# Kernel optimization log

Measured on AMD Instinct MI355X. Metric: run time of the kernel, lower is better.

## Reference

```python
import jax, jax.numpy as jnp
import numpy as np

H = 64
N_NODES = 12000
N_EDGES = 50000


def setup_inputs() -> dict:
    key = jax.random.key(0)
    ks = jax.random.split(key, 16)
    s = 1.0 / np.sqrt(H)
    inp = {
        "node": jax.random.normal(ks[0], (N_NODES, H), jnp.float32),
        "edge": jax.random.normal(ks[1], (N_EDGES, H), jnp.float32),
        "hidden_feats": jax.random.normal(ks[2], (N_NODES, H), jnp.float32),
        "src": jax.random.randint(ks[3], (N_EDGES,), 0, N_NODES, jnp.int32),
        "dst": jax.random.randint(ks[4], (N_EDGES,), 0, N_NODES, jnp.int32),
        # edge_network: Linear(H, 2H) -> ReLU -> Linear(2H, H*H)
        "W1": jax.random.uniform(ks[5], (2 * H, H), jnp.float32, -s, s),
        "b1": jax.random.uniform(ks[6], (2 * H,), jnp.float32, -s, s),
        "W2": jax.random.uniform(ks[7], (H * H, 2 * H), jnp.float32, -1 / np.sqrt(2 * H), 1 / np.sqrt(2 * H)),
        "b2": jax.random.uniform(ks[8], (H * H,), jnp.float32, -1 / np.sqrt(2 * H), 1 / np.sqrt(2 * H)),
        # GRUCell params (torch layout: [3H, H], gate order r,z,n)
        "W_ih": jax.random.uniform(ks[9], (3 * H, H), jnp.float32, -s, s),
        "W_hh": jax.random.uniform(ks[10], (3 * H, H), jnp.float32, -s, s),
        "b_ih": jax.random.uniform(ks[11], (3 * H,), jnp.float32, -s, s),
        "b_hh": jax.random.uniform(ks[12], (3 * H,), jnp.float32, -s, s),
        # LayerNorm params
        "gamma": jnp.ones((H,), jnp.float32),
        "beta": jnp.zeros((H,), jnp.float32),
    }
    return inp


def _gru_cell(x, h, W_ih, W_hh, b_ih, b_hh):
    gi = x @ W_ih.T + b_ih  # [N, 3H]
    gh = h @ W_hh.T + b_hh  # [N, 3H]
    r = jax.nn.sigmoid(gi[:, :H] + gh[:, :H])
    z = jax.nn.sigmoid(gi[:, H:2 * H] + gh[:, H:2 * H])
    n = jnp.tanh(gi[:, 2 * H:] + r * gh[:, 2 * H:])
    return (1.0 - z) * n + z * h


def reference(node, edge, hidden_feats, src, dst, W1, b1, W2, b2,
              W_ih, W_hh, b_ih, b_hh, gamma, beta):
    n_nodes = node.shape[0]
    # edge network -> per-edge [H,H] weight matrices
    eh = jax.nn.relu(edge @ W1.T + b1)                      # [E, 2H]
    Wedge = (eh @ W2.T + b2).reshape(-1, H, H)              # [E, H, H]
    # gather src feats, per-edge matmul (row-vector @ matrix), scatter-sum to dst
    msg = jnp.einsum('eh,ehk->ek', node[src], Wedge)        # [E, H]
    agg = jax.ops.segment_sum(msg, dst, num_segments=n_nodes)  # [N, H]
    new_node_feats = jax.nn.relu(agg)
    out = _gru_cell(new_node_feats, hidden_feats, W_ih, W_hh, b_ih, b_hh)
    # LayerNorm (eps=1e-5)
    mu = jnp.mean(out, axis=-1, keepdims=True)
    var = jnp.var(out, axis=-1, keepdims=True)
    out = (out - mu) * jax.lax.rsqrt(var + 1e-5) * gamma + beta
    return out
```

## Files before the change

kernel.cpp:

```cpp
#include <hip/hip_runtime.h>

#define H 64
#define NEDGE 50000
#define NNODE 12000
#define EPAD 50176

typedef _Float16 f16;
typedef _Float16 h8 __attribute__((ext_vector_type(8)));
typedef float f4 __attribute__((ext_vector_type(4)));

#define O_EDGEH 0ull
#define O_W2G   6422528ull
#define O_W1G   7471104ull
#define O_WG    7487488ull
#define O_NB    7553024ull
#define O_AGG   10625024ull

__device__ __forceinline__ void async16(const void* g, void* l) {
  __builtin_amdgcn_global_load_lds((const __attribute__((address_space(1))) void*)g,
                                   (__attribute__((address_space(3))) void*)l, 16, 0, 0);
}

__global__ __launch_bounds__(256) void k_prep(const float* __restrict__ edge, const float* __restrict__ W1,
                                              const float* __restrict__ W2, const float* __restrict__ b2,
                                              const float* __restrict__ node,
                                              const float* __restrict__ Wih, const float* __restrict__ Whh,
                                              f16* __restrict__ edgeh, f16* __restrict__ w1g, f16* __restrict__ w2g,
                                              f16* __restrict__ wg, float* __restrict__ nb) {
  int bid = blockIdx.x;
  int t = threadIdx.x;
  if (bid < 1568) {
    long id8 = (long)bid * 256 + t;
    long e = id8 >> 3;
    int c = (int)(id8 & 7) * 8;
    h8 o = {};
    if (e < NEDGE) {
      const float* p = edge + e * 64 + c;
      f4 v0 = *(const f4*)p, v1 = *(const f4*)(p + 4);
#pragma unroll
      for (int j = 0; j < 4; ++j) { o[j] = (f16)v0[j]; o[4 + j] = (f16)v1[j]; }
    }
    *(h8*)(edgeh + e * 64 + c) = o;
    return;
  }
  if (bid < 3616) {
    int id = (bid - 1568) * 256 + t;
    int ii = id & 7, l = (id >> 3) & 63, t4 = (id >> 9) & 3, s = (id >> 11) & 3, h = id >> 13;
    int n = t4 * 16 + (l & 15), j = s * 32 + ((l >> 4) << 3) + ii;
    w2g[id] = (f16)W2[(h * 64 + n) * 128 + j];
    return;
  }
  if (bid < 3648) {
    int id = (bid - 3616) * 256 + t;
    int ii = id & 7, l = (id >> 3) & 63, tt = (id >> 9) & 7, s = id >> 12;
    int n = tt * 16 + (l & 15), k = s * 32 + ((l >> 4) << 3) + ii;
    w1g[id] = (f16)W1[n * 64 + k];
    return;
  }
  if (bid < 3776) {
    int id = (bid - 3648) * 256 + t;
    int ii = id & 7, l = (id >> 3) & 63, tt = (id >> 9) & 15, s = id >> 13;
    int k = s * 32 + ((l >> 4) << 3) + ii, n = tt * 16 + (l & 15);
    float v;
    if (n < 128) v = (k < 64) ? Wih[n * 64 + k] : Whh[n * 64 + (k - 64)];
    else if (n < 192) v = (k < 64) ? Wih[n * 64 + k] : 0.f;
    else v = (k < 64) ? 0.f : Whh[(n - 64) * 64 + (k - 64)];
    wg[id] = (f16)v;
    return;
  }
  __shared__ float bs[64][65];
  __shared__ float xs[64][65];
  int n0 = (bid - 3776) * 64;
#pragma unroll
  for (int it = 0; it < 16; ++it) {
    int idx = t + it * 256;
    int rr = idx >> 6, cc = idx & 63;
    bs[rr][cc] = b2[idx];
    int nn = n0 + rr;
    xs[rr][cc] = (nn < NNODE) ? node[(long)nn * 64 + cc] : 0.f;
  }
  __syncthreads();
  int f0 = (t & 15) * 4, e0 = (t >> 4) * 4;
  float acc[4][4] = {};
#pragma unroll 4
  for (int k = 0; k < 64; ++k) {
    f4 w = *(const f4*)&bs[k][f0];
#pragma unroll
    for (int i = 0; i < 4; ++i) {
      float x = xs[e0 + i][k];
      acc[i][0] = fmaf(x, w[0], acc[i][0]); acc[i][1] = fmaf(x, w[1], acc[i][1]);
      acc[i][2] = fmaf(x, w[2], acc[i][2]); acc[i][3] = fmaf(x, w[3], acc[i][3]);
    }
  }
#pragma unroll
  for (int i = 0; i < 4; ++i) {
    int nn = n0 + e0 + i;
    if (nn < NNODE)
#pragma unroll
      for (int j = 0; j < 4; ++j) nb[(long)nn * 64 + f0 + j] = acc[i][j];
  }
}

__global__ __launch_bounds__(256, 3) void k_msg(const float* __restrict__ node,
                                                const int* __restrict__ src, const int* __restrict__ dst,
                                                const f16* __restrict__ edgeh, const f16* __restrict__ w1g,
                                                const f16* __restrict__ w2g, const float* __restrict__ b1,
                                                const float* __restrict__ nbt, float* __restrict__ agg) {
  __shared__ __align__(16) f16 est[64 * 8 * 8];
  __shared__ __align__(16) f16 eh_s[64 * 16 * 8];
  __shared__ __align__(16) f16 vT2[64 * 8 * 8];
  __shared__ int ssrc[64];
  __shared__ int sdst[64];
  __shared__ float b1s[128];

  int t = threadIdx.x;
  int e_base = blockIdx.x * 64;

  if (t < 64) {
    int eg = e_base + t;
    bool valid = eg < NEDGE;
    ssrc[t] = valid ? src[eg] : 0;
    sdst[t] = valid ? dst[eg] : 0;
  }
  if (t >= 128) b1s[t - 128] = b1[t - 128];
  {
    const char* ehb = (const char*)edgeh;
#pragma unroll
    for (int r = 0; r < 2; ++r) {
      int idx = r * 256 + t;
      int e = idx >> 3, c1 = idx & 7;
      int c = c1 ^ (e & 7);
      async16(ehb + ((long)(e_base + e) * 8 + c) * 16, (char*)est + idx * 16);
    }
  }
  {
    int e = t >> 2, q = t & 3;
    int eg = e_base + e;
    int si = (eg < NEDGE) ? src[eg] : 0;
    const f4* nr = (const f4*)(node + (long)si * 64 + q * 16);
    f4 a0 = nr[0], a1 = nr[1], a2 = nr[2], a3 = nr[3];
    h8 p0, p1;
#pragma unroll
    for (int m = 0; m < 4; ++m) {
      p0[m] = (f16)a0[m]; p0[4 + m] = (f16)a1[m];
      p1[m] = (f16)a2[m]; p1[4 + m] = (f16)a3[m];
    }
    int g0 = (q * 2) ^ (e & 7), g1 = (q * 2 + 1) ^ (e & 7);
    *(h8*)(vT2 + (e * 8 + g0) * 8) = p0;
    *(h8*)(vT2 + (e * 8 + g1) * 8) = p1;
  }
  __syncthreads();

  int wave = t >> 6, lane = t & 63;
  int l15 = lane & 15, lq = lane >> 4;

  {
    h8 afr[4][2];
#pragma unroll
    for (int g = 0; g < 4; ++g) {
      int e = g * 16 + l15;
#pragma unroll
      for (int s = 0; s < 2; ++s) {
        int c = (s * 4 + lq) ^ (e & 7);
        afr[g][s] = *(const h8*)(est + (e * 8 + c) * 8);
      }
    }
    h8 bfr[2][2];
#pragma unroll
    for (int s = 0; s < 2; ++s)
#pragma unroll
      for (int j = 0; j < 2; ++j)
        bfr[s][j] = *(const h8*)(w1g + ((s * 8 + wave * 2 + j) * 64 + lane) * 8);
    f4 acc_eh[4][2];
#pragma unroll
    for (int g = 0; g < 4; ++g) { acc_eh[g][0] = (f4){0,0,0,0}; acc_eh[g][1] = (f4){0,0,0,0}; }
#pragma unroll
    for (int s = 0; s < 2; ++s)
#pragma unroll
      for (int g = 0; g < 4; ++g)
#pragma unroll
        for (int j = 0; j < 2; ++j)
          acc_eh[g][j] = __builtin_amdgcn_mfma_f32_16x16x32_f16(afr[g][s], bfr[s][j], acc_eh[g][j], 0, 0, 0);
#pragma unroll
    for (int g = 0; g < 4; ++g)
#pragma unroll
      for (int j = 0; j < 2; ++j) {
        int n = wave * 32 + j * 16 + l15;
        int jg = n >> 3;
#pragma unroll
        for (int r = 0; r < 4; ++r) {
          int e = g * 16 + lq * 4 + r;
          float val = fmaxf(acc_eh[g][j][r] + b1s[n], 0.f);
          eh_s[(e * 16 + (jg ^ (e & 15))) * 8 + (n & 7)] = (f16)val;
        }
      }
  }
  __syncthreads();

  h8 ehreg[4][4];
#pragma unroll
  for (int g = 0; g < 4; ++g) {
    int e = g * 16 + l15;
#pragma unroll
    for (int s = 0; s < 4; ++s) {
      int jg = (s * 4 + lq) ^ (e & 15);
      ehreg[g][s] = *(const h8*)(eh_s + (e * 16 + jg) * 8);
    }
  }

  f4 acc[4];
#pragma unroll
  for (int g = 0; g < 4; ++g) acc[g] = (f4){0.f, 0.f, 0.f, 0.f};

  const char* w2b = (const char*)w2g + wave * 1024 + lane * 16;
  h8 cur0 = *(const h8*)(w2b);
  h8 cur1 = *(const h8*)(w2b + 4096);
  h8 cur2 = *(const h8*)(w2b + 8192);
  h8 cur3 = *(const h8*)(w2b + 12288);

#pragma unroll 1
  for (int hb = 0; hb < 8; ++hb) {
    h8 vh8[4];
#pragma unroll
    for (int g = 0; g < 4; ++g) {
      int e = g * 16 + l15;
      vh8[g] = *(const h8*)(vT2 + (e * 8 + (hb ^ (e & 7))) * 8);
    }
#pragma unroll
    for (int hh = 0; hh < 8; ++hh) {
      int h = hb * 8 + hh;
      const char* gp = w2b + (long)(h + 1) * 16384;
      h8 pf0 = *(const h8*)(gp);
      h8 pf1 = *(const h8*)(gp + 4096);
      h8 pf2 = *(const h8*)(gp + 8192);
      h8 pf3 = *(const h8*)(gp + 12288);
      f16 vs;
#pragma unroll
      for (int g = 0; g < 4; ++g) {
        vs = vh8[g][hh];
        h8 a = ehreg[g][0] * vs;
        acc[g] = __builtin_amdgcn_mfma_f32_16x16x32_f16(a, cur0, acc[g], 0, 0, 0);
        a = ehreg[g][1] * vs;
        acc[g] = __builtin_amdgcn_mfma_f32_16x16x32_f16(a, cur1, acc[g], 0, 0, 0);
        a = ehreg[g][2] * vs;
        acc[g] = __builtin_amdgcn_mfma_f32_16x16x32_f16(a, cur2, acc[g], 0, 0, 0);
        a = ehreg[g][3] * vs;
        acc[g] = __builtin_amdgcn_mfma_f32_16x16x32_f16(a, cur3, acc[g], 0, 0, 0);
      }
      cur0 = pf0; cur1 = pf1; cur2 = pf2; cur3 = pf3;
    }
  }

  int n = wave * 16 + l15;
#pragma unroll
  for (int g = 0; g < 4; ++g)
#pragma unroll
    for (int r = 0; r < 4; ++r) {
      int el = g * 16 + lq * 4 + r;
      if (e_base + el < NEDGE) {
        float v = acc[g][r] + nbt[(long)ssrc[el] * 64 + n];
        atomicAdd(&agg[(long)sdst[el] * 64 + n], v);
      }
    }
}

__global__ __launch_bounds__(256) void k_node(const float* __restrict__ agg, const float* __restrict__ hid,
                                              const f16* __restrict__ wg,
                                              const float* __restrict__ bih, const float* __restrict__ bhh,
                                              const float* __restrict__ gamma, const float* __restrict__ beta,
                                              float* __restrict__ out) {
  __shared__ __align__(16) f16 xh_s[128 * 136];
  __shared__ float bsum[128], bin_s[64], bhn_s[64], gam_s[64], bet_s[64];
  int t = threadIdx.x;
  int n0 = blockIdx.x * 128;

  if (t < 128) bsum[t] = bih[t] + bhh[t];
  else if (t < 192) bin_s[t - 128] = bih[t];
  else bhn_s[t - 192] = bhh[t - 64];
  if (t < 64) gam_s[t] = gamma[t];
  else if (t < 128) bet_s[t - 64] = beta[t - 64];

  {
    int m = t >> 1, half = t & 1;
    int mg = n0 + m;
    bool vld = mg < NNODE;
    const float* sp = half ? (hid + (long)mg * 64) : (agg + (long)mg * 64);
#pragma unroll
    for (int jj = 0; jj < 8; ++jj) {
      f4 v0 = {0,0,0,0}, v1 = {0,0,0,0};
      if (vld) { v0 = *(const f4*)(sp + jj * 8); v1 = *(const f4*)(sp + jj * 8 + 4); }
      h8 pk;
#pragma unroll
      for (int m2 = 0; m2 < 4; ++m2) {
        pk[m2] = (f16)(half ? v0[m2] : fmaxf(v0[m2], 0.f));
        pk[4 + m2] = (f16)(half ? v1[m2] : fmaxf(v1[m2], 0.f));
      }
      *(h8*)(xh_s + m * 136 + half * 64 + jj * 8) = pk;
    }
  }
  __syncthreads();

  int wave = t >> 6, lane = t & 63;
  int l15 = lane & 15, lq = lane >> 4;

  f4 acc[2][16];
#pragma unroll
  for (int g = 0; g < 2; ++g)
#pragma unroll
    for (int tt = 0; tt < 16; ++tt) acc[g][tt] = (f4){0.f, 0.f, 0.f, 0.f};

#pragma unroll
  for (int s = 0; s < 4; ++s) {
    h8 a0 = *(const h8*)(xh_s + (wave * 32 + l15) * 136 + s * 32 + lq * 8);
    h8 a1 = *(const h8*)(xh_s + (wave * 32 + 16 + l15) * 136 + s * 32 + lq * 8);
#pragma unroll
    for (int tt = 0; tt < 16; ++tt) {
      h8 b = *(const h8*)(wg + ((s * 16 + tt) * 64 + lane) * 8);
      acc[0][tt] = __builtin_amdgcn_mfma_f32_16x16x32_f16(a0, b, acc[0][tt], 0, 0, 0);
      acc[1][tt] = __builtin_amdgcn_mfma_f32_16x16x32_f16(a1, b, acc[1][tt], 0, 0, 0);
    }
  }

#pragma unroll
  for (int g = 0; g < 2; ++g)
#pragma unroll
    for (int r = 0; r < 4; ++r) {
      int mg = n0 + wave * 32 + g * 16 + lq * 4 + r;
      bool vld = mg < NNODE;
      float o[4], ssum = 0.f, s2 = 0.f;
#pragma unroll
      for (int t0 = 0; t0 < 4; ++t0) {
        int f = t0 * 16 + l15;
        float rpre = acc[g][t0][r] + bsum[f];
        float zpre = acc[g][4 + t0][r] + bsum[64 + f];
        float ginv = acc[g][8 + t0][r] + bin_s[f];
        float ghnv = acc[g][12 + t0][r] + bhn_s[f];
        float rr = 1.f / (1.f + __expf(-rpre));
        float zz = 1.f / (1.f + __expf(-zpre));
        float hv = vld ? hid[(long)mg * 64 + f] : 0.f;
        float nn = tanhf(ginv + rr * ghnv);
        float oo = (1.f - zz) * nn + zz * hv;
        o[t0] = oo; ssum += oo; s2 += oo * oo;
      }
#pragma unroll
      for (int d = 1; d < 16; d <<= 1) {
        ssum += __shfl_xor(ssum, d);
        s2 += __shfl_xor(s2, d);
      }
      float mu = ssum * (1.f / 64.f);
      float var = s2 * (1.f / 64.f) - mu * mu;
      float rstd = rsqrtf(var + 1e-5f);
      if (vld)
#pragma unroll
        for (int t0 = 0; t0 < 4; ++t0) {
          int f = t0 * 16 + l15;
          out[(long)mg * 64 + f] = (o[t0] - mu) * rstd * gam_s[f] + bet_s[f];
        }
    }
}

extern "C" void kernel_launch(void* const* d_in, const int* in_sizes, int n_in,
                              void* d_out, int out_size, void* d_ws, size_t ws_size,
                              hipStream_t stream) {
  const float* node = (const float*)d_in[0];
  const float* edge = (const float*)d_in[1];
  const float* hid = (const float*)d_in[2];
  const int* src = (const int*)d_in[3];
  const int* dst = (const int*)d_in[4];
  const float* W1 = (const float*)d_in[5];
  const float* b1 = (const float*)d_in[6];
  const float* W2 = (const float*)d_in[7];
  const float* b2 = (const float*)d_in[8];
  const float* Wih = (const float*)d_in[9];
  const float* Whh = (const float*)d_in[10];
  const float* bih = (const float*)d_in[11];
  const float* bhh = (const float*)d_in[12];
  const float* gamma = (const float*)d_in[13];
  const float* beta = (const float*)d_in[14];

  char* ws = (char*)d_ws;
  f16* edgeh = (f16*)(ws + O_EDGEH);
  f16* w2g = (f16*)(ws + O_W2G);
  f16* w1g = (f16*)(ws + O_W1G);
  f16* wg = (f16*)(ws + O_WG);
  float* nb = (float*)(ws + O_NB);
  float* agg = (float*)(ws + O_AGG);

  hipMemsetAsync(agg, 0, (size_t)NNODE * 64 * sizeof(float), stream);
  k_prep<<<3964, 256, 0, stream>>>(edge, W1, W2, b2, node, Wih, Whh, edgeh, w1g, w2g, wg, nb);
  k_msg<<<784, 256, 0, stream>>>(node, src, dst, edgeh, w1g, w2g, b1, nb, agg);
  k_node<<<94, 256, 0, stream>>>(agg, hid, wg, bih, bhh, gamma, beta, (float*)d_out);
}
```

Before: 219.5 us.

## Restructure k_msg to 256 edges per block with LDS double-buffered W2 tiles

```diff
diff --git a/kernel.cpp b/kernel.cpp
--- a/kernel.cpp
+++ b/kernel.cpp
@@ -26,11 +26,16 @@
                                               const float* __restrict__ node,
                                               const float* __restrict__ Wih, const float* __restrict__ Whh,
                                               f16* __restrict__ edgeh, f16* __restrict__ w1g, f16* __restrict__ w2g,
-                                              f16* __restrict__ wg, float* __restrict__ nb) {
+                                              f16* __restrict__ wg, float* __restrict__ nb, float* __restrict__ agg) {
   int bid = blockIdx.x;
   int t = threadIdx.x;
-  if (bid < 1568) {
-    long id8 = (long)bid * 256 + t;
+  if (bid < 750) {
+    int id = bid * 256 + t;
+    *(f4*)(agg + (long)id * 4) = (f4){0.f, 0.f, 0.f, 0.f};
+    return;
+  }
+  if (bid < 2318) {
+    long id8 = (long)(bid - 750) * 256 + t;
     long e = id8 >> 3;
     int c = (int)(id8 & 7) * 8;
     h8 o = {};
@@ -43,22 +48,22 @@
     *(h8*)(edgeh + e * 64 + c) = o;
     return;
   }
-  if (bid < 3616) {
-    int id = (bid - 1568) * 256 + t;
+  if (bid < 4366) {
+    int id = (bid - 2318) * 256 + t;
     int ii = id & 7, l = (id >> 3) & 63, t4 = (id >> 9) & 3, s = (id >> 11) & 3, h = id >> 13;
     int n = t4 * 16 + (l & 15), j = s * 32 + ((l >> 4) << 3) + ii;
     w2g[id] = (f16)W2[(h * 64 + n) * 128 + j];
     return;
   }
-  if (bid < 3648) {
-    int id = (bid - 3616) * 256 + t;
+  if (bid < 4398) {
+    int id = (bid - 4366) * 256 + t;
     int ii = id & 7, l = (id >> 3) & 63, tt = (id >> 9) & 7, s = id >> 12;
     int n = tt * 16 + (l & 15), k = s * 32 + ((l >> 4) << 3) + ii;
     w1g[id] = (f16)W1[n * 64 + k];
     return;
   }
-  if (bid < 3776) {
-    int id = (bid - 3648) * 256 + t;
+  if (bid < 4526) {
+    int id = (bid - 4398) * 256 + t;
     int ii = id & 7, l = (id >> 3) & 63, tt = (id >> 9) & 15, s = id >> 13;
     int k = s * 32 + ((l >> 4) << 3) + ii, n = tt * 16 + (l & 15);
     float v;
@@ -70,7 +75,7 @@
   }
   __shared__ float bs[64][65];
   __shared__ float xs[64][65];
-  int n0 = (bid - 3776) * 64;
+  int n0 = (bid - 4526) * 64;
 #pragma unroll
   for (int it = 0; it < 16; ++it) {
     int idx = t + it * 256;
@@ -101,167 +106,161 @@
   }
 }
 
-__global__ __launch_bounds__(256, 3) void k_msg(const float* __restrict__ node,
+__global__ __launch_bounds__(256, 2) void k_msg(const float* __restrict__ node,
                                                 const int* __restrict__ src, const int* __restrict__ dst,
                                                 const f16* __restrict__ edgeh, const f16* __restrict__ w1g,
                                                 const f16* __restrict__ w2g, const float* __restrict__ b1,
                                                 const float* __restrict__ nbt, float* __restrict__ agg) {
-  __shared__ __align__(16) f16 est[64 * 8 * 8];
-  __shared__ __align__(16) f16 eh_s[64 * 16 * 8];
-  __shared__ __align__(16) f16 vT2[64 * 8 * 8];
-  __shared__ int ssrc[64];
-  __shared__ int sdst[64];
-  __shared__ float b1s[128];
+  __shared__ __align__(16) char lds[104960];
+  f16* eh_s = (f16*)lds;
+  char* bbuf = lds;
+  int* ssrc = (int*)(lds + 102400);
+  int* sdst = (int*)(lds + 103424);
+  float* b1s = (float*)(lds + 104448);
 
   int t = threadIdx.x;
-  int e_base = blockIdx.x * 64;
-
-  if (t < 64) {
+  int e_base = blockIdx.x * 256;
+
+  {
     int eg = e_base + t;
     bool valid = eg < NEDGE;
-    ssrc[t] = valid ? src[eg] : 0;
+    int si = valid ? src[eg] : 0;
+    ssrc[t] = si;
     sdst[t] = valid ? dst[eg] : 0;
-  }
-  if (t >= 128) b1s[t - 128] = b1[t - 128];
-  {
-    const char* ehb = (const char*)edgeh;
-#pragma unroll
-    for (int r = 0; r < 2; ++r) {
-      int idx = r * 256 + t;
-      int e = idx >> 3, c1 = idx & 7;
-      int c = c1 ^ (e & 7);
-      async16(ehb + ((long)(e_base + e) * 8 + c) * 16, (char*)est + idx * 16);
-    }
-  }
-  {
-    int e = t >> 2, q = t & 3;
-    int eg = e_base + e;
-    int si = (eg < NEDGE) ? src[eg] : 0;
-    const f4* nr = (const f4*)(node + (long)si * 64 + q * 16);
-    f4 a0 = nr[0], a1 = nr[1], a2 = nr[2], a3 = nr[3];
-    h8 p0, p1;
-#pragma unroll
-    for (int m = 0; m < 4; ++m) {
-      p0[m] = (f16)a0[m]; p0[4 + m] = (f16)a1[m];
-      p1[m] = (f16)a2[m]; p1[4 + m] = (f16)a3[m];
-    }
-    int g0 = (q * 2) ^ (e & 7), g1 = (q * 2 + 1) ^ (e & 7);
-    *(h8*)(vT2 + (e * 8 + g0) * 8) = p0;
-    *(h8*)(vT2 + (e * 8 + g1) * 8) = p1;
+    if (t < 128) b1s[t] = b1[t];
+    const f4* nr = (const f4*)(node + (long)si * 64);
+    f16* vrow = (f16*)(lds + 65536 + t * 144);
+#pragma unroll
+    for (int b = 0; b < 8; ++b) {
+      f4 v0 = nr[b * 2], v1 = nr[b * 2 + 1];
+      h8 pk;
+#pragma unroll
+      for (int m = 0; m < 4; ++m) { pk[m] = (f16)v0[m]; pk[4 + m] = (f16)v1[m]; }
+      *(h8*)(vrow + b * 8) = pk;
+    }
   }
   __syncthreads();
 
   int wave = t >> 6, lane = t & 63;
   int l15 = lane & 15, lq = lane >> 4;
+  int ew0 = wave * 64;
 
   {
     h8 afr[4][2];
 #pragma unroll
-    for (int g = 0; g < 4; ++g) {
-      int e = g * 16 + l15;
-#pragma unroll
-      for (int s = 0; s < 2; ++s) {
-        int c = (s * 4 + lq) ^ (e & 7);
-        afr[g][s] = *(const h8*)(est + (e * 8 + c) * 8);
-      }
-    }
-    h8 bfr[2][2];
-#pragma unroll
-    for (int s = 0; s < 2; ++s)
-#pragma unroll
-      for (int j = 0; j < 2; ++j)
-        bfr[s][j] = *(const h8*)(w1g + ((s * 8 + wave * 2 + j) * 64 + lane) * 8);
-    f4 acc_eh[4][2];
-#pragma unroll
-    for (int g = 0; g < 4; ++g) { acc_eh[g][0] = (f4){0,0,0,0}; acc_eh[g][1] = (f4){0,0,0,0}; }
-#pragma unroll
-    for (int s = 0; s < 2; ++s)
+    for (int g = 0; g < 4; ++g)
+#pragma unroll
+      for (int s = 0; s < 2; ++s)
+        afr[g][s] = *(const h8*)(edgeh + (long)(e_base + ew0 + g * 16 + l15) * 64 + s * 32 + lq * 8);
+#pragma unroll
+    for (int nh = 0; nh < 2; ++nh) {
+      h8 bfr[2][4];
+#pragma unroll
+      for (int s = 0; s < 2; ++s)
+#pragma unroll
+        for (int tt = 0; tt < 4; ++tt)
+          bfr[s][tt] = *(const h8*)(w1g + ((s * 8 + nh * 4 + tt) * 64 + lane) * 8);
+      f4 acc_eh[4][4];
 #pragma unroll
       for (int g = 0; g < 4; ++g)
 #pragma unroll
-        for (int j = 0; j < 2; ++j)
-          acc_eh[g][j] = __builtin_amdgcn_mfma_f32_16x16x32_f16(afr[g][s], bfr[s][j], acc_eh[g][j], 0, 0, 0);
+        for (int tt = 0; tt < 4; ++tt) acc_eh[g][tt] = (f4){0.f, 0.f, 0.f, 0.f};
+#pragma unroll
+      for (int s = 0; s < 2; ++s)
+#pragma unroll
+        for (int g = 0; g < 4; ++g)
+#pragma unroll
+          for (int tt = 0; tt < 4; ++tt)
+            acc_eh[g][tt] = __builtin_amdgcn_mfma_f32_16x16x32_f16(afr[g][s], bfr[s][tt], acc_eh[g][tt], 0, 0, 0);
+#pragma unroll
+      for (int g = 0; g < 4; ++g)
+#pragma unroll
+        for (int tt = 0; tt < 4; ++tt) {
+          int n = (nh * 4 + tt) * 16 + l15;
+          int jg = n >> 3;
+#pragma unroll
+          for (int r = 0; r < 4; ++r) {
+            int e = ew0 + g * 16 + lq * 4 + r;
+            float val = fmaxf(acc_eh[g][tt][r] + b1s[n], 0.f);
+            eh_s[(e * 16 + (jg ^ (e & 15))) * 8 + (n & 7)] = (f16)val;
+          }
+        }
+    }
+  }
+  __syncthreads();
+
+  h8 ehreg[4][4];
+#pragma unroll
+  for (int g = 0; g < 4; ++g) {
+    int e = ew0 + g * 16 + l15;
+#pragma unroll
+    for (int s = 0; s < 4; ++s)
+      ehreg[g][s] = *(const h8*)(eh_s + (e * 16 + ((s * 4 + lq) ^ (e & 15))) * 8);
+  }
+  __syncthreads();
+
+  const char* w2b = (const char*)w2g;
+#pragma unroll
+  for (int r = 0; r < 8; ++r) async16(w2b + r * 4096 + t * 16, bbuf + r * 4096 + t * 16);
+
+  f4 acc[4][4];
+#pragma unroll
+  for (int g = 0; g < 4; ++g)
+#pragma unroll
+    for (int tt = 0; tt < 4; ++tt) acc[g][tt] = (f4){0.f, 0.f, 0.f, 0.f};
+
+#pragma unroll 1
+  for (int hpb = 0; hpb < 8; ++hpb) {
+    h8 vh8[4];
 #pragma unroll
     for (int g = 0; g < 4; ++g)
-#pragma unroll
-      for (int j = 0; j < 2; ++j) {
-        int n = wave * 32 + j * 16 + l15;
-        int jg = n >> 3;
-#pragma unroll
-        for (int r = 0; r < 4; ++r) {
-          int e = g * 16 + lq * 4 + r;
-          float val = fmaxf(acc_eh[g][j][r] + b1s[n], 0.f);
-          eh_s[(e * 16 + (jg ^ (e & 15))) * 8 + (n & 7)] = (f16)val;
+      vh8[g] = *(const h8*)(lds + 65536 + (ew0 + g * 16 + l15) * 144 + hpb * 16);
+#pragma unroll
+    for (int hpi = 0; hpi < 4; ++hpi) {
+      int hp = hpb * 4 + hpi;
+      __syncthreads();
+      {
+        const char* gsrc = w2b + (long)(hp + 1) * 32768;
+        char* ldst = bbuf + ((hp + 1) & 1) * 32768;
+#pragma unroll
+        for (int r = 0; r < 8; ++r) async16(gsrc + r * 4096 + t * 16, ldst + r * 4096 + t * 16);
+      }
+      const char* bp = bbuf + (hp & 1) * 32768;
+#pragma unroll
+      for (int sub = 0; sub < 2; ++sub) {
+        const f16* bc = (const f16*)(bp + sub * 16384);
+        const int hh = hpi * 2 + sub;
+#pragma unroll
+        for (int s = 0; s < 4; ++s) {
+          h8 bf[4];
+#pragma unroll
+          for (int tt = 0; tt < 4; ++tt)
+            bf[tt] = *(const h8*)(bc + ((s * 4 + tt) * 64 + lane) * 8);
+#pragma unroll
+          for (int g = 0; g < 4; ++g) {
+            h8 a = ehreg[g][s] * vh8[g][hh];
+#pragma unroll
+            for (int tt = 0; tt < 4; ++tt)
+              acc[g][tt] = __builtin_amdgcn_mfma_f32_16x16x32_f16(a, bf[tt], acc[g][tt], 0, 0, 0);
+          }
         }
       }
-  }
-  __syncthreads();
-
-  h8 ehreg[4][4];
-#pragma unroll
-  for (int g = 0; g < 4; ++g) {
-    int e = g * 16 + l15;
-#pragma unroll
-    for (int s = 0; s < 4; ++s) {
-      int jg = (s * 4 + lq) ^ (e & 15);
-      ehreg[g][s] = *(const h8*)(eh_s + (e * 16 + jg) * 8);
-    }
-  }
-
-  f4 acc[4];
-#pragma unroll
-  for (int g = 0; g < 4; ++g) acc[g] = (f4){0.f, 0.f, 0.f, 0.f};
-
-  const char* w2b = (const char*)w2g + wave * 1024 + lane * 16;
-  h8 cur0 = *(const h8*)(w2b);
-  h8 cur1 = *(const h8*)(w2b + 4096);
-  h8 cur2 = *(const h8*)(w2b + 8192);
-  h8 cur3 = *(const h8*)(w2b + 12288);
-
-#pragma unroll 1
-  for (int hb = 0; hb < 8; ++hb) {
-    h8 vh8[4];
-#pragma unroll
-    for (int g = 0; g < 4; ++g) {
-      int e = g * 16 + l15;
-      vh8[g] = *(const h8*)(vT2 + (e * 8 + (hb ^ (e & 7))) * 8);
-    }
-#pragma unroll
-    for (int hh = 0; hh < 8; ++hh) {
-      int h = hb * 8 + hh;
-      const char* gp = w2b + (long)(h + 1) * 16384;
-      h8 pf0 = *(const h8*)(gp);
-      h8 pf1 = *(const h8*)(gp + 4096);
-      h8 pf2 = *(const h8*)(gp + 8192);
-      h8 pf3 = *(const h8*)(gp + 12288);
-      f16 vs;
-#pragma unroll
-      for (int g = 0; g < 4; ++g) {
-        vs = vh8[g][hh];
-        h8 a = ehreg[g][0] * vs;
-        acc[g] = __builtin_amdgcn_mfma_f32_16x16x32_f16(a, cur0, acc[g], 0, 0, 0);
-        a = ehreg[g][1] * vs;
-        acc[g] = __builtin_amdgcn_mfma_f32_16x16x32_f16(a, cur1, acc[g], 0, 0, 0);
-        a = ehreg[g][2] * vs;
-        acc[g] = __builtin_amdgcn_mfma_f32_16x16x32_f16(a, cur2, acc[g], 0, 0, 0);
-        a = ehreg[g][3] * vs;
-        acc[g] = __builtin_amdgcn_mfma_f32_16x16x32_f16(a, cur3, acc[g], 0, 0, 0);
-      }
-      cur0 = pf0; cur1 = pf1; cur2 = pf2; cur3 = pf3;
-    }
-  }
-
-  int n = wave * 16 + l15;
+    }
+  }
+
 #pragma unroll
   for (int g = 0; g < 4; ++g)
 #pragma unroll
-    for (int r = 0; r < 4; ++r) {
-      int el = g * 16 + lq * 4 + r;
-      if (e_base + el < NEDGE) {
-        float v = acc[g][r] + nbt[(long)ssrc[el] * 64 + n];
-        atomicAdd(&agg[(long)sdst[el] * 64 + n], v);
-      }
-    }
+    for (int tt = 0; tt < 4; ++tt)
+#pragma unroll
+      for (int r = 0; r < 4; ++r) {
+        int el = ew0 + g * 16 + lq * 4 + r;
+        if (e_base + el < NEDGE) {
+          int n = tt * 16 + l15;
+          float v = acc[g][tt][r] + nbt[(long)ssrc[el] * 64 + n];
+          atomicAdd(&agg[(long)sdst[el] * 64 + n], v);
+        }
+      }
 }
 
 __global__ __launch_bounds__(256) void k_node(const float* __restrict__ agg, const float* __restrict__ hid,
@@ -287,7 +286,7 @@
     const float* sp = half ? (hid + (long)mg * 64) : (agg + (long)mg * 64);
 #pragma unroll
     for (int jj = 0; jj < 8; ++jj) {
-      f4 v0 = {0,0,0,0}, v1 = {0,0,0,0};
+      f4 v0 = {0, 0, 0, 0}, v1 = {0, 0, 0, 0};
       if (vld) { v0 = *(const f4*)(sp + jj * 8); v1 = *(const f4*)(sp + jj * 8 + 4); }
       h8 pk;
 #pragma unroll
@@ -386,8 +385,7 @@
   float* nb = (float*)(ws + O_NB);
   float* agg = (float*)(ws + O_AGG);
 
-  hipMemsetAsync(agg, 0, (size_t)NNODE * 64 * sizeof(float), stream);
-  k_prep<<<3964, 256, 0, stream>>>(edge, W1, W2, b2, node, Wih, Whh, edgeh, w1g, w2g, wg, nb);
-  k_msg<<<784, 256, 0, stream>>>(node, src, dst, edgeh, w1g, w2g, b1, nb, agg);
+  k_prep<<<4714, 256, 0, stream>>>(edge, W1, W2, b2, node, Wih, Whh, edgeh, w1g, w2g, wg, nb, agg);
+  k_msg<<<196, 256, 0, stream>>>(node, src, dst, edgeh, w1g, w2g, b1, nb, agg);
   k_node<<<94, 256, 0, stream>>>(agg, hid, wg, bih, bhh, gamma, beta, (float*)d_out);
 }
```

Measured after the change: 214.2 us. -2.4%, faster.
